# Kernel optimization log

Hardware: AMD Instinct MI355X
Metric: run time of the kernel (lower is better)

The kernel has to match this reference:

```python
import jax, jax.numpy as jnp
import numpy as np
from jax import lax

MAX_DISP = 4  # correlation window radius -> 9x9 = 81 offsets


def setup_inputs() -> dict:
    key = jax.random.key(0)
    k1, k2 = jax.random.split(key)
    B, C, H, W = 4, 256, 128, 128
    x_1 = jax.random.normal(k1, (B, C, H, W), dtype=jnp.float32)
    x_2 = jax.random.normal(k2, (B, C, H, W), dtype=jnp.float32)
    return {"x_1": x_1, "x_2": x_2}


def reference(x_1, x_2):
    # FlowNet-style correlation: for each displacement (dy, dx) in [-4, 4]^2,
    # out[b, (dy+4)*9 + (dx+4), y, x] = mean_c x1[b,c,y,x] * x2[b,c,y+dy,x+dx]
    # with zero padding of x2 (normalized by C, as in the original CUDA kernel).
    B, C, H, W = x_1.shape
    pad = jnp.pad(x_2, ((0, 0), (0, 0), (MAX_DISP, MAX_DISP), (MAX_DISP, MAX_DISP)))
    outs = []
    for dy in range(2 * MAX_DISP + 1):
        for dx in range(2 * MAX_DISP + 1):
            shifted = lax.dynamic_slice(pad, (0, 0, dy, dx), (B, C, H, W))
            outs.append(jnp.mean(x_1 * shifted, axis=1))  # [B, H, W]
    return jnp.stack(outs, axis=1)  # [B, 81, H, W]
```

## Files before the change

### kernel.cpp

```cpp
#include <hip/hip_runtime.h>


#define MD 4
constexpr int Bc = 4, Cc = 256, Hc = 128, Wc = 128;
constexpr int TH = 16, TW = 16;
constexpr int NDY = 3;
constexpr int CC = 4;
constexpr int SROWS = TH + NDY - 1;
constexpr int SCOLS = TW + 2 * MD;
constexpr int RSC = 48;
constexpr int CH_STRIDE = SROWS * RSC;
constexpr int BUF_DW = CC * CH_STRIDE;
constexpr int NF4 = CC * SROWS * (SCOLS / 4);
constexpr int NTHR = 192;
constexpr int NSLOT = 3;
constexpr int NK = Cc / CC;

__global__ __launch_bounds__(NTHR, 4)
void corr_kernel(const float* __restrict__ x1, const float* __restrict__ x2,
                 float* __restrict__ out)
{
    __shared__ float stg[2 * BUF_DW];

    const int tid  = threadIdx.x;
    const int w    = tid >> 6;
    const int lane = tid & 63;
    const int gy   = lane >> 2;
    const int gx   = lane & 3;

    const int bid  = blockIdx.x;
    const int q    = bid / 24;
    const int r    = bid - q * 24;
    const int g    = r >> 3;
    const int t    = q * 8 + (r & 7);
    const int tx = t & 7;
    const int ty = (t >> 3) & 7;
    const int bb = t >> 6;
    const int x0 = tx * TW, y0 = ty * TH;
    const int rowbase = y0 + 3 * g - MD;

    int  s_goff[NSLOT], s_loff[NSLOT];
    bool s_val[NSLOT], s_act[NSLOT];
    #pragma unroll
    for (int s = 0; s < NSLOT; ++s) {
        int idx = tid + s * NTHR;
        bool active = idx < NF4;
        int i2  = active ? idx : 0;
        int cl  = i2 / (SROWS * 6);
        int rem = i2 - cl * (SROWS * 6);
        int rr  = rem / 6;
        int gc  = rem - rr * 6;
        int yy  = rowbase + rr;
        int xx  = x0 - 4 + 4 * gc;
        s_act[s]  = active;
        s_val[s]  = active && ((unsigned)yy < (unsigned)Hc) && ((unsigned)xx < (unsigned)(Wc - 3));
        s_goff[s] = cl * (Hc * Wc) + yy * Wc + xx;
        s_loff[s] = cl * CH_STRIDE + rr * RSC + 4 * gc;
    }

    const float* x2b = x2 + (size_t)bb * Cc * Hc * Wc;
    const float* x1b = x1 + (((size_t)bb * Cc) * Hc + (y0 + gy)) * Wc + x0 + 4 * gx;

    float acc[9][4];
    #pragma unroll
    for (int dx = 0; dx < 9; ++dx)
        #pragma unroll
        for (int p = 0; p < 4; ++p) acc[dx][p] = 0.f;

    const float4 f40 = make_float4(0.f, 0.f, 0.f, 0.f);
    float4 nf[NSLOT];

    #pragma unroll
    for (int s = 0; s < NSLOT; ++s) {
        nf[s] = f40;
        if (s_val[s]) nf[s] = *(const float4*)(x2b + s_goff[s]);
    }
    #pragma unroll
    for (int s = 0; s < NSLOT; ++s)
        if (s_act[s]) *(float4*)(&stg[s_loff[s]]) = nf[s];

    for (int k = 0; k < NK; ++k) {
        const int pb = k & 1;
        if (k + 1 < NK) {
            const int gof = (k + 1) * CC * Hc * Wc;
            #pragma unroll
            for (int s = 0; s < NSLOT; ++s) {
                nf[s] = f40;
                if (s_val[s]) nf[s] = *(const float4*)(x2b + gof + s_goff[s]);
            }
        }
        __syncthreads();
        #pragma unroll
        for (int cl = 0; cl < CC; ++cl) {
            const int c = k * CC + cl;
            const float4 a4 = *(const float4*)(x1b + c * (Hc * Wc));
            const float* rowp = &stg[pb * BUF_DW + cl * CH_STRIDE + (gy + w) * RSC + 4 * gx];
            const float4 q0 = *(const float4*)(rowp);
            const float4 q1 = *(const float4*)(rowp + 4);
            const float4 q2 = *(const float4*)(rowp + 8);
            const float v[12] = {q0.x, q0.y, q0.z, q0.w,
                                 q1.x, q1.y, q1.z, q1.w,
                                 q2.x, q2.y, q2.z, q2.w};
            const float a[4] = {a4.x, a4.y, a4.z, a4.w};
            #pragma unroll
            for (int dx = 0; dx < 9; ++dx)
                #pragma unroll
                for (int p = 0; p < 4; ++p)
                    acc[dx][p] += a[p] * v[dx + p];
        }
        if (k + 1 < NK) {
            const int lb = ((k + 1) & 1) * BUF_DW;
            #pragma unroll
            for (int s = 0; s < NSLOT; ++s)
                if (s_act[s]) *(float4*)(&stg[lb + s_loff[s]]) = nf[s];
        }
    }

    const float inv = 1.0f / (float)Cc;
    float* ob = out + (((size_t)bb * 81 + (3 * g + w) * 9) * Hc + (y0 + gy)) * Wc + x0 + 4 * gx;
    #pragma unroll
    for (int dx = 0; dx < 9; ++dx) {
        float4 st = make_float4(acc[dx][0] * inv, acc[dx][1] * inv,
                                acc[dx][2] * inv, acc[dx][3] * inv);
        *(float4*)(ob + dx * (Hc * Wc)) = st;
    }
}

extern "C" void kernel_launch(void* const* d_in, const int* in_sizes, int n_in,
                              void* d_out, int out_size, void* d_ws, size_t ws_size,
                              hipStream_t stream) {
    const float* x1 = (const float*)d_in[0];
    const float* x2 = (const float*)d_in[1];
    float* out = (float*)d_out;
    dim3 grid(3 * 8 * 8 * Bc), block(NTHR);
    corr_kernel<<<grid, block, 0, stream>>>(x1, x2, out);
}
```

Before: 201.1 us.

## Stage x1 and x2 via async global-to-LDS loads with triple buffering

Replaces register-staged x2 loads with global_load_lds direct-to-LDS DMA, and also stages x1 tiles into LDS instead of reading them from global per channel. Uses a 3-deep buffer ring with explicit waitcnt and barrier, prefetching two chunks ahead. Out-of-bounds slots read from a zeroed workspace page, which requires a memset before each launch. LDS use grows and launch bounds drop to 2 blocks per CU, which may reduce occupancy.

```diff
diff --git a/kernel.cpp b/kernel.cpp
--- a/kernel.cpp
+++ b/kernel.cpp
@@ -1,26 +1,34 @@
 #include <hip/hip_runtime.h>
+#include <stdint.h>
 
 
 #define MD 4
 constexpr int Bc = 4, Cc = 256, Hc = 128, Wc = 128;
+constexpr int HW = Hc * Wc;
 constexpr int TH = 16, TW = 16;
-constexpr int NDY = 3;
 constexpr int CC = 4;
-constexpr int SROWS = TH + NDY - 1;
-constexpr int SCOLS = TW + 2 * MD;
-constexpr int RSC = 48;
-constexpr int CH_STRIDE = SROWS * RSC;
-constexpr int BUF_DW = CC * CH_STRIDE;
-constexpr int NF4 = CC * SROWS * (SCOLS / 4);
-constexpr int NTHR = 192;
-constexpr int NSLOT = 3;
+constexpr int SROWS = 18, SCOLS = 24;
+constexpr int X2_SLOTS = CC * SROWS * (SCOLS / 4);
+constexpr int X2_PAD   = 448;
+constexpr int X1_SLOTS = CC * TH * (TW / 4);
+constexpr int SL_TOT   = 768;
+constexpr int BUF_DW   = SL_TOT * 4;
+constexpr int X1OFF    = X2_PAD * 4;
+constexpr int NTHR  = 192;
+constexpr int NSLOT = 4;
 constexpr int NK = Cc / CC;
 
-__global__ __launch_bounds__(NTHR, 4)
+__device__ __forceinline__ void async16(const void* g, const void* l) {
+    __builtin_amdgcn_global_load_lds(
+        (const __attribute__((address_space(1))) unsigned int*)g,
+        (__attribute__((address_space(3))) unsigned int*)l, 16, 0, 0);
+}
+
+__global__ __launch_bounds__(NTHR, 2)
 void corr_kernel(const float* __restrict__ x1, const float* __restrict__ x2,
-                 float* __restrict__ out)
+                 const float* __restrict__ zpage, float* __restrict__ out)
 {
-    __shared__ float stg[2 * BUF_DW];
+    __shared__ float stg[3 * BUF_DW];
 
     const int tid  = threadIdx.x;
     const int w    = tid >> 6;
@@ -28,38 +36,46 @@
     const int gy   = lane >> 2;
     const int gx   = lane & 3;
 
-    const int bid  = blockIdx.x;
-    const int q    = bid / 24;
-    const int r    = bid - q * 24;
-    const int g    = r >> 3;
-    const int t    = q * 8 + (r & 7);
-    const int tx = t & 7;
-    const int ty = (t >> 3) & 7;
-    const int bb = t >> 6;
+    const int bid = blockIdx.x;
+    const int q   = bid / 24;
+    const int r0  = bid - q * 24;
+    const int g   = r0 >> 3;
+    const int t   = q * 8 + (r0 & 7);
+    const int tx = t & 7, ty = (t >> 3) & 7, bb = t >> 6;
     const int x0 = tx * TW, y0 = ty * TH;
     const int rowbase = y0 + 3 * g - MD;
 
-    int  s_goff[NSLOT], s_loff[NSLOT];
-    bool s_val[NSLOT], s_act[NSLOT];
+    const char* sp[NSLOT];
+    int sstep[NSLOT], sloff[NSLOT];
+    const size_t cbase = (size_t)bb * Cc * HW;
     #pragma unroll
     for (int s = 0; s < NSLOT; ++s) {
-        int idx = tid + s * NTHR;
-        bool active = idx < NF4;
-        int i2  = active ? idx : 0;
-        int cl  = i2 / (SROWS * 6);
-        int rem = i2 - cl * (SROWS * 6);
-        int rr  = rem / 6;
-        int gc  = rem - rr * 6;
-        int yy  = rowbase + rr;
-        int xx  = x0 - 4 + 4 * gc;
-        s_act[s]  = active;
-        s_val[s]  = active && ((unsigned)yy < (unsigned)Hc) && ((unsigned)xx < (unsigned)(Wc - 3));
-        s_goff[s] = cl * (Hc * Wc) + yy * Wc + xx;
-        s_loff[s] = cl * CH_STRIDE + rr * RSC + 4 * gc;
+        const int slot = tid + s * NTHR;
+        sloff[s] = slot * 4;
+        if (slot < X2_SLOTS) {
+            const int cl  = slot / 108;
+            const int rem = slot - cl * 108;
+            const int rr  = rem / 6;
+            const int gc  = rem - rr * 6;
+            const int yy  = rowbase + rr;
+            const int xx  = x0 - 4 + 4 * gc;
+            const bool valid = ((unsigned)yy < (unsigned)Hc) && ((unsigned)xx <= (unsigned)(Wc - 4));
+            sp[s]    = valid ? (const char*)(x2 + cbase + (size_t)cl * HW + yy * Wc + xx)
+                             : (const char*)zpage;
+            sstep[s] = valid ? (int)(CC * HW * sizeof(float)) : 0;
+        } else if (slot < X2_PAD) {
+            sp[s] = (const char*)zpage;  sstep[s] = 0;
+        } else if (slot < X2_PAD + X1_SLOTS) {
+            const int j   = slot - X2_PAD;
+            const int cl  = j >> 6;
+            const int py  = (j >> 2) & 15;
+            const int pxg = j & 3;
+            sp[s]    = (const char*)(x1 + cbase + (size_t)cl * HW + (y0 + py) * Wc + x0 + 4 * pxg);
+            sstep[s] = (int)(CC * HW * sizeof(float));
+        } else {
+            sp[s] = (const char*)zpage;  sstep[s] = 0;
+        }
     }
-
-    const float* x2b = x2 + (size_t)bb * Cc * Hc * Wc;
-    const float* x1b = x1 + (((size_t)bb * Cc) * Hc + (y0 + gy)) * Wc + x0 + 4 * gx;
 
     float acc[9][4];
     #pragma unroll
@@ -67,34 +83,37 @@
         #pragma unroll
         for (int p = 0; p < 4; ++p) acc[dx][p] = 0.f;
 
-    const float4 f40 = make_float4(0.f, 0.f, 0.f, 0.f);
-    float4 nf[NSLOT];
-
     #pragma unroll
     for (int s = 0; s < NSLOT; ++s) {
-        nf[s] = f40;
-        if (s_val[s]) nf[s] = *(const float4*)(x2b + s_goff[s]);
+        async16(sp[s], (const void*)(&stg[0 * BUF_DW] + sloff[s]));
+        sp[s] += sstep[s];
     }
     #pragma unroll
-    for (int s = 0; s < NSLOT; ++s)
-        if (s_act[s]) *(float4*)(&stg[s_loff[s]]) = nf[s];
+    for (int s = 0; s < NSLOT; ++s) {
+        async16(sp[s], (const void*)(&stg[1 * BUF_DW] + sloff[s]));
+        sp[s] += sstep[s];
+    }
 
+    int bc = 0;
     for (int k = 0; k < NK; ++k) {
-        const int pb = k & 1;
-        if (k + 1 < NK) {
-            const int gof = (k + 1) * CC * Hc * Wc;
+        if (k == NK - 1) __builtin_amdgcn_s_waitcnt(0x0F70);
+        else             __builtin_amdgcn_s_waitcnt(0x0F74);
+        __builtin_amdgcn_s_barrier();
+        __builtin_amdgcn_sched_barrier(0);
+        if (k + 2 < NK) {
+            int b2 = bc + 2; if (b2 >= 3) b2 -= 3;
+            float* bp2 = &stg[b2 * BUF_DW];
             #pragma unroll
             for (int s = 0; s < NSLOT; ++s) {
-                nf[s] = f40;
-                if (s_val[s]) nf[s] = *(const float4*)(x2b + gof + s_goff[s]);
+                async16(sp[s], (const void*)(bp2 + sloff[s]));
+                sp[s] += sstep[s];
             }
         }
-        __syncthreads();
+        const float* bp = &stg[bc * BUF_DW];
         #pragma unroll
         for (int cl = 0; cl < CC; ++cl) {
-            const int c = k * CC + cl;
-            const float4 a4 = *(const float4*)(x1b + c * (Hc * Wc));
-            const float* rowp = &stg[pb * BUF_DW + cl * CH_STRIDE + (gy + w) * RSC + 4 * gx];
+            const float4 a4 = *(const float4*)(bp + X1OFF + cl * 256 + gy * 16 + 4 * gx);
+            const float* rowp = bp + cl * (SROWS * SCOLS) + (gy + w) * SCOLS + 4 * gx;
             const float4 q0 = *(const float4*)(rowp);
             const float4 q1 = *(const float4*)(rowp + 4);
             const float4 q2 = *(const float4*)(rowp + 8);
@@ -108,12 +127,7 @@
                 for (int p = 0; p < 4; ++p)
                     acc[dx][p] += a[p] * v[dx + p];
         }
-        if (k + 1 < NK) {
-            const int lb = ((k + 1) & 1) * BUF_DW;
-            #pragma unroll
-            for (int s = 0; s < NSLOT; ++s)
-                if (s_act[s]) *(float4*)(&stg[lb + s_loff[s]]) = nf[s];
-        }
+        if (++bc == 3) bc = 0;
     }
 
     const float inv = 1.0f / (float)Cc;
@@ -122,7 +136,7 @@
     for (int dx = 0; dx < 9; ++dx) {
         float4 st = make_float4(acc[dx][0] * inv, acc[dx][1] * inv,
                                 acc[dx][2] * inv, acc[dx][3] * inv);
-        *(float4*)(ob + dx * (Hc * Wc)) = st;
+        *(float4*)(ob + dx * HW) = st;
     }
 }
 
@@ -132,6 +146,7 @@
     const float* x1 = (const float*)d_in[0];
     const float* x2 = (const float*)d_in[1];
     float* out = (float*)d_out;
+    hipMemsetAsync(d_ws, 0, 64, stream);
     dim3 grid(3 * 8 * 8 * Bc), block(NTHR);
-    corr_kernel<<<grid, block, 0, stream>>>(x1, x2, out);
+    corr_kernel<<<grid, block, 0, stream>>>(x1, x2, (const float*)d_ws, out);
 }
```

Result: no change. 204.2 us (+1.5%).
